# Performance work log

Measured on AMD Instinct MI355X. Metric: run time of the kernel, lower is better.

Reference implementation:

```python
import jax, jax.numpy as jnp
import numpy as np

N_NODES = 100000
DEG = 16
D_IN = 128
D_OUT = 128


def setup_inputs() -> dict:
    key = jax.random.key(0)
    k1, k2, k3, k4, k5, k6 = jax.random.split(key, 6)
    neighbours = jax.random.randint(k1, (N_NODES, DEG), 0, N_NODES, dtype=jnp.int64 if jax.config.jax_enable_x64 else jnp.int32)
    shape_features = jax.random.normal(k2, (N_NODES, D_IN), dtype=jnp.float32)
    scale = 1.0 / np.sqrt(D_IN)
    W1 = jax.random.normal(k3, (D_OUT, D_IN), dtype=jnp.float32) * scale
    b1 = jax.random.normal(k4, (D_OUT,), dtype=jnp.float32) * scale
    W2 = jax.random.normal(k5, (D_OUT, D_IN), dtype=jnp.float32) * scale
    b2 = jax.random.normal(k6, (D_OUT,), dtype=jnp.float32) * scale
    return {"neighbours": neighbours, "shape_features": shape_features,
            "W1": W1, "b1": b1, "W2": W2, "b2": b2}


def reference(neighbours, shape_features, W1, b1, W2, b2):
    # linear1(x): x @ W1^T + b1  -> [N, D_OUT]
    out1 = jnp.einsum('nd,od->no', shape_features, W1) + b1
    # per-node neighbor gather + sum (vectorized form of the Python loop)
    # gathered: [N, DEG, D_IN], aggr: [N, D_IN]
    aggr = shape_features[neighbours].sum(axis=1)
    out = out1 + jnp.einsum('nd,od->no', aggr, W2) + b2
    return jax.nn.relu(out)
```

## Files before the change

kernel.cpp:

```cpp
#include <hip/hip_runtime.h>
#include <stdint.h>


#define N_NODES 100000
#define DEG 16

typedef __attribute__((ext_vector_type(8))) short short8;
typedef __attribute__((ext_vector_type(4))) float floatx4;

static __device__ __forceinline__ unsigned short f2bf(float f) {
  union { float f; uint32_t u; } v; v.f = f;
  uint32_t u = v.u;
  return (unsigned short)((u + 0x7fffu + ((u >> 16) & 1u)) >> 16);
}
static __device__ __forceinline__ float bf2f(uint32_t bits16) {
  union { uint32_t u; float f; } v; v.u = bits16 << 16; return v.f;
}

__global__ __launch_bounds__(256) void k_convert(const float* __restrict__ x,
                                                 unsigned short* __restrict__ Xb,
                                                 const float* __restrict__ W1, const float* __restrict__ b1,
                                                 const float* __restrict__ W2, const float* __restrict__ b2,
                                                 unsigned short* __restrict__ Bt, float* __restrict__ bias) {
  int b = blockIdx.x;
  if (b < 12500) {
    int t = b * 256 + threadIdx.x;
    int n = t >> 5, c4 = t & 31;
    float4 v = *(const float4*)(x + (size_t)n * 128 + (size_t)c4 * 4);
    ushort4 o;
    o.x = f2bf(v.x); o.y = f2bf(v.y); o.z = f2bf(v.z); o.w = f2bf(v.w);
    *(ushort4*)(Xb + (size_t)n * 128 + (size_t)c4 * 4) = o;
  } else {
    int t = (b - 12500) * 256 + threadIdx.x;
    int o = t >> 8, k = t & 255;
    float v = (k < 128) ? W1[o * 128 + k] : W2[o * 128 + (k - 128)];
    Bt[t] = f2bf(v);
    if (t < 128) bias[t] = b1[t] + b2[t];
  }
}

__global__ __launch_bounds__(256, 8) void k_fused(const int* __restrict__ nbrs,
                                                  const unsigned short* __restrict__ Xb,
                                                  const unsigned short* __restrict__ Bt,
                                                  const float* __restrict__ bias,
                                                  float* __restrict__ out) {
  __shared__ uint4 aggr4[512];
  char* aggr = (char*)aggr4;
  const int tid = threadIdx.x;
  const int lane = tid & 63;
  const int w = tid >> 6;
  const int q16 = lane >> 4, c16 = lane & 15;
  const int tile = blockIdx.x * 32;
  const char* Xbb = (const char*)Xb;
  const char* Btb = (const char*)Bt;

  float bcol[2];
#pragma unroll
  for (int ni = 0; ni < 2; ++ni) bcol[ni] = bias[w * 32 + ni * 16 + c16];

  int base = (tile + w * 8) * DEG;
  int midx0 = nbrs[base + lane];
  int midx1 = nbrs[base + 64 + lane];

  for (int q = 0; q < 8; ++q) {
    int midx = (q < 4) ? midx0 : midx1;
    int flat = (q & 3) * 16 + q16;
    float a8[8] = {0.f, 0.f, 0.f, 0.f, 0.f, 0.f, 0.f, 0.f};
#pragma unroll
    for (int i = 0; i < 4; ++i) {
      int nb = __shfl(midx, flat + i * 4);
      uint4 pv = *(const uint4*)(Xbb + (size_t)nb * 256 + c16 * 16);
      a8[0] += bf2f(pv.x & 0xffffu); a8[1] += bf2f(pv.x >> 16);
      a8[2] += bf2f(pv.y & 0xffffu); a8[3] += bf2f(pv.y >> 16);
      a8[4] += bf2f(pv.z & 0xffffu); a8[5] += bf2f(pv.z >> 16);
      a8[6] += bf2f(pv.w & 0xffffu); a8[7] += bf2f(pv.w >> 16);
    }
#pragma unroll
    for (int k = 0; k < 8; ++k) {
      a8[k] += __shfl_xor(a8[k], 16);
      a8[k] += __shfl_xor(a8[k], 32);
    }
    if (lane < 16) {
      int row = w * 8 + q;
      uint4 wv;
      wv.x = (uint32_t)f2bf(a8[0]) | ((uint32_t)f2bf(a8[1]) << 16);
      wv.y = (uint32_t)f2bf(a8[2]) | ((uint32_t)f2bf(a8[3]) << 16);
      wv.z = (uint32_t)f2bf(a8[4]) | ((uint32_t)f2bf(a8[5]) << 16);
      wv.w = (uint32_t)f2bf(a8[6]) | ((uint32_t)f2bf(a8[7]) << 16);
      *(uint4*)(aggr + row * 256 + ((c16 ^ (row & 7)) * 16)) = wv;
    }
  }

  __syncthreads();

  floatx4 acc[2][2];
#pragma unroll
  for (int mi = 0; mi < 2; ++mi)
#pragma unroll
    for (int ni = 0; ni < 2; ++ni) acc[mi][ni] = (floatx4){0.f, 0.f, 0.f, 0.f};

#pragma unroll
  for (int kt = 0; kt < 8; ++kt) {
    short8 a[2], b[2];
#pragma unroll
    for (int mi = 0; mi < 2; ++mi) {
      int row = mi * 16 + c16;
      if (kt < 4) {
        a[mi] = *(const short8*)(Xbb + (size_t)(tile + row) * 256 + kt * 64 + q16 * 16);
      } else {
        int slot = (((kt - 4) * 4 + q16) ^ (row & 7)) * 16;
        a[mi] = *(const short8*)(aggr + row * 256 + slot);
      }
    }
#pragma unroll
    for (int ni = 0; ni < 2; ++ni) {
      int o = w * 32 + ni * 16 + c16;
      b[ni] = *(const short8*)(Btb + (size_t)o * 512 + kt * 64 + q16 * 16);
    }
    __builtin_amdgcn_s_setprio(1);
    acc[0][0] = __builtin_amdgcn_mfma_f32_16x16x32_bf16(a[0], b[0], acc[0][0], 0, 0, 0);
    acc[0][1] = __builtin_amdgcn_mfma_f32_16x16x32_bf16(a[0], b[1], acc[0][1], 0, 0, 0);
    acc[1][0] = __builtin_amdgcn_mfma_f32_16x16x32_bf16(a[1], b[0], acc[1][0], 0, 0, 0);
    acc[1][1] = __builtin_amdgcn_mfma_f32_16x16x32_bf16(a[1], b[1], acc[1][1], 0, 0, 0);
    __builtin_amdgcn_s_setprio(0);
  }

#pragma unroll
  for (int mi = 0; mi < 2; ++mi) {
    int rbase = tile + mi * 16 + q16 * 4;
#pragma unroll
    for (int r = 0; r < 4; ++r) {
      float* orow = out + (size_t)(rbase + r) * 128 + w * 32 + c16;
#pragma unroll
      for (int ni = 0; ni < 2; ++ni) {
        float vv = acc[mi][ni][r] + bcol[ni];
        orow[ni * 16] = vv > 0.f ? vv : 0.f;
      }
    }
  }
}

extern "C" void kernel_launch(void* const* d_in, const int* in_sizes, int n_in,
                              void* d_out, int out_size, void* d_ws, size_t ws_size,
                              hipStream_t stream) {
  const int* nbrs  = (const int*)d_in[0];
  const float* x   = (const float*)d_in[1];
  const float* W1  = (const float*)d_in[2];
  const float* b1  = (const float*)d_in[3];
  const float* W2  = (const float*)d_in[4];
  const float* b2  = (const float*)d_in[5];
  float* out = (float*)d_out;

  unsigned short* Xb = (unsigned short*)d_ws;
  unsigned short* Bt = Xb + (size_t)N_NODES * 128;
  float* bias = (float*)(Bt + 128 * 256);

  k_convert<<<12628, 256, 0, stream>>>(x, Xb, W1, b1, W2, b2, Bt, bias);
  k_fused<<<3125, 256, 0, stream>>>(nbrs, Xb, Bt, bias, out);
}
```

Baseline: 177.9 us.

## Double-buffer neighbour gathers and stage self tile into LDS via async loads

Software-pipelines the neighbour gather by issuing the next quad's global loads into one register buffer while summing the previous one. It also copies the block's own 32-row X tile into a swizzled LDS buffer with global_load_lds at kernel start, so the MFMA loop reads A operands from LDS instead of global memory. The occupancy hint drops from 8 to 6 blocks per CU to make room for the extra registers and the doubled LDS, which can reduce latency hiding across waves.

Result: faster. 170.6 us (-4.1%).

```diff
diff --git a/kernel.cpp b/kernel.cpp
--- a/kernel.cpp
+++ b/kernel.cpp
@@ -39,13 +39,14 @@
   }
 }
 
-__global__ __launch_bounds__(256, 8) void k_fused(const int* __restrict__ nbrs,
+__global__ __launch_bounds__(256, 6) void k_fused(const int* __restrict__ nbrs,
                                                   const unsigned short* __restrict__ Xb,
                                                   const unsigned short* __restrict__ Bt,
                                                   const float* __restrict__ bias,
                                                   float* __restrict__ out) {
-  __shared__ uint4 aggr4[512];
-  char* aggr = (char*)aggr4;
+  __shared__ uint4 lds4[1024];
+  char* xbuf = (char*)lds4;
+  char* aggr = (char*)lds4 + 8192;
   const int tid = threadIdx.x;
   const int lane = tid & 63;
   const int w = tid >> 6;
@@ -53,6 +54,16 @@
   const int tile = blockIdx.x * 32;
   const char* Xbb = (const char*)Xb;
   const char* Btb = (const char*)Bt;
+
+#pragma unroll
+  for (int i = 0; i < 2; ++i) {
+    int g = w * 2 + i;
+    int row = 4 * g + (lane >> 4);
+    const char* src = Xbb + (size_t)(tile + row) * 256 + ((size_t)((lane & 15) ^ (row & 7))) * 16;
+    __builtin_amdgcn_global_load_lds((const __attribute__((address_space(1))) uint32_t*)src,
+                                     (__attribute__((address_space(3))) uint32_t*)(xbuf + g * 1024),
+                                     16, 0, 0);
+  }
 
   float bcol[2];
 #pragma unroll
@@ -62,14 +73,21 @@
   int midx0 = nbrs[base + lane];
   int midx1 = nbrs[base + 64 + lane];
 
-  for (int q = 0; q < 8; ++q) {
+  uint4 pA[4], pB[4];
+  auto ISSUE = [&](int q, uint4* buf) {
     int midx = (q < 4) ? midx0 : midx1;
     int flat = (q & 3) * 16 + q16;
+#pragma unroll
+    for (int i = 0; i < 4; ++i) {
+      int nb = __shfl(midx, flat + i * 4);
+      buf[i] = *(const uint4*)(Xbb + (size_t)nb * 256 + c16 * 16);
+    }
+  };
+  auto CONSUME = [&](int q, uint4* buf) {
     float a8[8] = {0.f, 0.f, 0.f, 0.f, 0.f, 0.f, 0.f, 0.f};
 #pragma unroll
     for (int i = 0; i < 4; ++i) {
-      int nb = __shfl(midx, flat + i * 4);
-      uint4 pv = *(const uint4*)(Xbb + (size_t)nb * 256 + c16 * 16);
+      uint4 pv = buf[i];
       a8[0] += bf2f(pv.x & 0xffffu); a8[1] += bf2f(pv.x >> 16);
       a8[2] += bf2f(pv.y & 0xffffu); a8[3] += bf2f(pv.y >> 16);
       a8[4] += bf2f(pv.z & 0xffffu); a8[5] += bf2f(pv.z >> 16);
@@ -89,7 +107,17 @@
       wv.w = (uint32_t)f2bf(a8[6]) | ((uint32_t)f2bf(a8[7]) << 16);
       *(uint4*)(aggr + row * 256 + ((c16 ^ (row & 7)) * 16)) = wv;
     }
-  }
+  };
+
+  ISSUE(0, pA);
+  ISSUE(1, pB); CONSUME(0, pA);
+  ISSUE(2, pA); CONSUME(1, pB);
+  ISSUE(3, pB); CONSUME(2, pA);
+  ISSUE(4, pA); CONSUME(3, pB);
+  ISSUE(5, pB); CONSUME(4, pA);
+  ISSUE(6, pA); CONSUME(5, pB);
+  ISSUE(7, pB); CONSUME(6, pA);
+  CONSUME(7, pB);
 
   __syncthreads();
 
@@ -101,16 +129,13 @@
 
 #pragma unroll
   for (int kt = 0; kt < 8; ++kt) {
+    const char* srcb = (kt < 4) ? xbuf : aggr;
+    int s = (kt & 3) * 4 + q16;
     short8 a[2], b[2];
 #pragma unroll
     for (int mi = 0; mi < 2; ++mi) {
       int row = mi * 16 + c16;
-      if (kt < 4) {
-        a[mi] = *(const short8*)(Xbb + (size_t)(tile + row) * 256 + kt * 64 + q16 * 16);
-      } else {
-        int slot = (((kt - 4) * 4 + q16) ^ (row & 7)) * 16;
-        a[mi] = *(const short8*)(aggr + row * 256 + slot);
-      }
+      a[mi] = *(const short8*)(srcb + row * 256 + ((s ^ (row & 7)) * 16));
     }
 #pragma unroll
     for (int ni = 0; ni < 2; ++ni) {
```

## Assign one node per 16-lane group in gather, dropping cross-lane reductions

Applied to the files above, without the earlier changes.

The neighbour gather now gives each 16-lane group a whole node and has it walk all 16 neighbours, instead of splitting one node's neighbours across four groups and combining partial sums with shuffles. This removes the xor-shuffle reductions and the lane<16 guarded writes, so all lanes store rows to shared memory. The high bf16 half is now unpacked with a mask instead of shift-then-shift. The trade-off is a longer serial chain of 16 loads per lane (two rounds instead of eight), which relies on memory-level parallelism from unrolling and may raise register pressure.

Measured after the change: 182.8 us. 1.03x slower.

```diff
diff --git a/kernel.cpp b/kernel.cpp
--- a/kernel.cpp
+++ b/kernel.cpp
@@ -13,8 +13,11 @@
   uint32_t u = v.u;
   return (unsigned short)((u + 0x7fffu + ((u >> 16) & 1u)) >> 16);
 }
-static __device__ __forceinline__ float bf2f(uint32_t bits16) {
-  union { uint32_t u; float f; } v; v.u = bits16 << 16; return v.f;
+static __device__ __forceinline__ float bflo(uint32_t u) {
+  union { uint32_t u; float f; } v; v.u = u << 16; return v.f;
+}
+static __device__ __forceinline__ float bfhi(uint32_t u) {
+  union { uint32_t u; float f; } v; v.u = u & 0xffff0000u; return v.f;
 }
 
 __global__ __launch_bounds__(256) void k_convert(const float* __restrict__ x,
@@ -49,7 +52,7 @@
   const int tid = threadIdx.x;
   const int lane = tid & 63;
   const int w = tid >> 6;
-  const int q16 = lane >> 4, c16 = lane & 15;
+  const int g = lane >> 4, c16 = lane & 15;
   const int tile = blockIdx.x * 32;
   const char* Xbb = (const char*)Xb;
   const char* Btb = (const char*)Bt;
@@ -58,37 +61,27 @@
 #pragma unroll
   for (int ni = 0; ni < 2; ++ni) bcol[ni] = bias[w * 32 + ni * 16 + c16];
 
-  int base = (tile + w * 8) * DEG;
-  int midx0 = nbrs[base + lane];
-  int midx1 = nbrs[base + 64 + lane];
-
-  for (int q = 0; q < 8; ++q) {
-    int midx = (q < 4) ? midx0 : midx1;
-    int flat = (q & 3) * 16 + q16;
+  const int nbase = (tile + w * 8) * DEG;
+#pragma unroll
+  for (int round = 0; round < 2; ++round) {
+    int midx = nbrs[nbase + round * 64 + lane];
     float a8[8] = {0.f, 0.f, 0.f, 0.f, 0.f, 0.f, 0.f, 0.f};
 #pragma unroll
-    for (int i = 0; i < 4; ++i) {
-      int nb = __shfl(midx, flat + i * 4);
+    for (int j = 0; j < DEG; ++j) {
+      int nb = __shfl(midx, g * 16 + j);
       uint4 pv = *(const uint4*)(Xbb + (size_t)nb * 256 + c16 * 16);
-      a8[0] += bf2f(pv.x & 0xffffu); a8[1] += bf2f(pv.x >> 16);
-      a8[2] += bf2f(pv.y & 0xffffu); a8[3] += bf2f(pv.y >> 16);
-      a8[4] += bf2f(pv.z & 0xffffu); a8[5] += bf2f(pv.z >> 16);
-      a8[6] += bf2f(pv.w & 0xffffu); a8[7] += bf2f(pv.w >> 16);
+      a8[0] += bflo(pv.x); a8[1] += bfhi(pv.x);
+      a8[2] += bflo(pv.y); a8[3] += bfhi(pv.y);
+      a8[4] += bflo(pv.z); a8[5] += bfhi(pv.z);
+      a8[6] += bflo(pv.w); a8[7] += bfhi(pv.w);
     }
-#pragma unroll
-    for (int k = 0; k < 8; ++k) {
-      a8[k] += __shfl_xor(a8[k], 16);
-      a8[k] += __shfl_xor(a8[k], 32);
-    }
-    if (lane < 16) {
-      int row = w * 8 + q;
-      uint4 wv;
-      wv.x = (uint32_t)f2bf(a8[0]) | ((uint32_t)f2bf(a8[1]) << 16);
-      wv.y = (uint32_t)f2bf(a8[2]) | ((uint32_t)f2bf(a8[3]) << 16);
-      wv.z = (uint32_t)f2bf(a8[4]) | ((uint32_t)f2bf(a8[5]) << 16);
-      wv.w = (uint32_t)f2bf(a8[6]) | ((uint32_t)f2bf(a8[7]) << 16);
-      *(uint4*)(aggr + row * 256 + ((c16 ^ (row & 7)) * 16)) = wv;
-    }
+    int row = w * 8 + round * 4 + g;
+    uint4 wv;
+    wv.x = (uint32_t)f2bf(a8[0]) | ((uint32_t)f2bf(a8[1]) << 16);
+    wv.y = (uint32_t)f2bf(a8[2]) | ((uint32_t)f2bf(a8[3]) << 16);
+    wv.z = (uint32_t)f2bf(a8[4]) | ((uint32_t)f2bf(a8[5]) << 16);
+    wv.w = (uint32_t)f2bf(a8[6]) | ((uint32_t)f2bf(a8[7]) << 16);
+    *(uint4*)(aggr + row * 256 + ((c16 ^ (row & 7)) * 16)) = wv;
   }
 
   __syncthreads();
@@ -106,16 +99,16 @@
     for (int mi = 0; mi < 2; ++mi) {
       int row = mi * 16 + c16;
       if (kt < 4) {
-        a[mi] = *(const short8*)(Xbb + (size_t)(tile + row) * 256 + kt * 64 + q16 * 16);
+        a[mi] = *(const short8*)(Xbb + (size_t)(tile + row) * 256 + kt * 64 + g * 16);
       } else {
-        int slot = (((kt - 4) * 4 + q16) ^ (row & 7)) * 16;
+        int slot = (((kt - 4) * 4 + g) ^ (row & 7)) * 16;
         a[mi] = *(const short8*)(aggr + row * 256 + slot);
       }
     }
 #pragma unroll
     for (int ni = 0; ni < 2; ++ni) {
       int o = w * 32 + ni * 16 + c16;
-      b[ni] = *(const short8*)(Btb + (size_t)o * 512 + kt * 64 + q16 * 16);
+      b[ni] = *(const short8*)(Btb + (size_t)o * 512 + kt * 64 + g * 16);
     }
     __builtin_amdgcn_s_setprio(1);
     acc[0][0] = __builtin_amdgcn_mfma_f32_16x16x32_bf16(a[0], b[0], acc[0][0], 0, 0, 0);
@@ -127,7 +120,7 @@
 
 #pragma unroll
   for (int mi = 0; mi < 2; ++mi) {
-    int rbase = tile + mi * 16 + q16 * 4;
+    int rbase = tile + mi * 16 + g * 4;
 #pragma unroll
     for (int r = 0; r < 4; ++r) {
       float* orow = out + (size_t)(rbase + r) * 128 + w * 32 + c16;
```

## Give each wave its own 16-row tile and drop block-level barrier

Applied to the files above, without the earlier changes.

Each wave now owns 16 output rows across all 128 output columns, with a private LDS slice for its aggregated neighbour rows. This removes the block-wide __syncthreads between the gather and MFMA phases, and each A fragment is reused across 8 MFMAs instead of 2. Blocks now cover 64 rows, so half as many blocks are launched, and occupancy is capped at 6 blocks per CU. The cost is that every wave reloads the full weight matrix from global or cache, and each wave holds more accumulator registers.

Measured after the change: 220.8 us. 1.24x slower.

```diff
diff --git a/kernel.cpp b/kernel.cpp
--- a/kernel.cpp
+++ b/kernel.cpp
@@ -39,103 +39,85 @@
   }
 }
 
-__global__ __launch_bounds__(256, 8) void k_fused(const int* __restrict__ nbrs,
+__global__ __launch_bounds__(256, 6) void k_fused(const int* __restrict__ nbrs,
                                                   const unsigned short* __restrict__ Xb,
                                                   const unsigned short* __restrict__ Bt,
                                                   const float* __restrict__ bias,
                                                   float* __restrict__ out) {
-  __shared__ uint4 aggr4[512];
-  char* aggr = (char*)aggr4;
+  __shared__ uint4 lds4[1024];
   const int tid = threadIdx.x;
   const int lane = tid & 63;
   const int w = tid >> 6;
-  const int q16 = lane >> 4, c16 = lane & 15;
-  const int tile = blockIdx.x * 32;
+  const int g = lane >> 4, c16 = lane & 15;
+  const int rb = blockIdx.x * 64 + w * 16;
+  if (rb >= N_NODES) return;
+  char* aggr = (char*)(lds4 + w * 256);
   const char* Xbb = (const char*)Xb;
   const char* Btb = (const char*)Bt;
 
-  float bcol[2];
+  float bcol[8];
 #pragma unroll
-  for (int ni = 0; ni < 2; ++ni) bcol[ni] = bias[w * 32 + ni * 16 + c16];
+  for (int nt = 0; nt < 8; ++nt) bcol[nt] = bias[nt * 16 + c16];
 
-  int base = (tile + w * 8) * DEG;
-  int midx0 = nbrs[base + lane];
-  int midx1 = nbrs[base + 64 + lane];
-
-  for (int q = 0; q < 8; ++q) {
-    int midx = (q < 4) ? midx0 : midx1;
-    int flat = (q & 3) * 16 + q16;
-    float a8[8] = {0.f, 0.f, 0.f, 0.f, 0.f, 0.f, 0.f, 0.f};
+  for (int qq = 0; qq < 4; ++qq) {
+    int mi_ = nbrs[(size_t)rb * DEG + qq * 64 + lane];
+    for (int qi = 0; qi < 4; ++qi) {
+      int q = qq * 4 + qi;
+      float a8[8] = {0.f, 0.f, 0.f, 0.f, 0.f, 0.f, 0.f, 0.f};
 #pragma unroll
-    for (int i = 0; i < 4; ++i) {
-      int nb = __shfl(midx, flat + i * 4);
-      uint4 pv = *(const uint4*)(Xbb + (size_t)nb * 256 + c16 * 16);
-      a8[0] += bf2f(pv.x & 0xffffu); a8[1] += bf2f(pv.x >> 16);
-      a8[2] += bf2f(pv.y & 0xffffu); a8[3] += bf2f(pv.y >> 16);
-      a8[4] += bf2f(pv.z & 0xffffu); a8[5] += bf2f(pv.z >> 16);
-      a8[6] += bf2f(pv.w & 0xffffu); a8[7] += bf2f(pv.w >> 16);
-    }
+      for (int i = 0; i < 4; ++i) {
+        int nb = __shfl(mi_, qi * 16 + i * 4 + g);
+        uint4 pv = *(const uint4*)(Xbb + (size_t)nb * 256 + c16 * 16);
+        a8[0] += bf2f(pv.x & 0xffffu); a8[1] += bf2f(pv.x >> 16);
+        a8[2] += bf2f(pv.y & 0xffffu); a8[3] += bf2f(pv.y >> 16);
+        a8[4] += bf2f(pv.z & 0xffffu); a8[5] += bf2f(pv.z >> 16);
+        a8[6] += bf2f(pv.w & 0xffffu); a8[7] += bf2f(pv.w >> 16);
+      }
 #pragma unroll
-    for (int k = 0; k < 8; ++k) {
-      a8[k] += __shfl_xor(a8[k], 16);
-      a8[k] += __shfl_xor(a8[k], 32);
-    }
-    if (lane < 16) {
-      int row = w * 8 + q;
-      uint4 wv;
-      wv.x = (uint32_t)f2bf(a8[0]) | ((uint32_t)f2bf(a8[1]) << 16);
-      wv.y = (uint32_t)f2bf(a8[2]) | ((uint32_t)f2bf(a8[3]) << 16);
-      wv.z = (uint32_t)f2bf(a8[4]) | ((uint32_t)f2bf(a8[5]) << 16);
-      wv.w = (uint32_t)f2bf(a8[6]) | ((uint32_t)f2bf(a8[7]) << 16);
-      *(uint4*)(aggr + row * 256 + ((c16 ^ (row & 7)) * 16)) = wv;
+      for (int k = 0; k < 8; ++k) {
+        a8[k] += __shfl_xor(a8[k], 16);
+        a8[k] += __shfl_xor(a8[k], 32);
+      }
+      if (lane < 16) {
+        uint4 wv;
+        wv.x = (uint32_t)f2bf(a8[0]) | ((uint32_t)f2bf(a8[1]) << 16);
+        wv.y = (uint32_t)f2bf(a8[2]) | ((uint32_t)f2bf(a8[3]) << 16);
+        wv.z = (uint32_t)f2bf(a8[4]) | ((uint32_t)f2bf(a8[5]) << 16);
+        wv.w = (uint32_t)f2bf(a8[6]) | ((uint32_t)f2bf(a8[7]) << 16);
+        *(uint4*)(aggr + q * 256 + ((c16 ^ (q & 7)) * 16)) = wv;
+      }
     }
   }
 
-  __syncthreads();
-
-  floatx4 acc[2][2];
+  floatx4 acc[8];
 #pragma unroll
-  for (int mi = 0; mi < 2; ++mi)
-#pragma unroll
-    for (int ni = 0; ni < 2; ++ni) acc[mi][ni] = (floatx4){0.f, 0.f, 0.f, 0.f};
+  for (int nt = 0; nt < 8; ++nt) acc[nt] = (floatx4){0.f, 0.f, 0.f, 0.f};
 
 #pragma unroll
   for (int kt = 0; kt < 8; ++kt) {
-    short8 a[2], b[2];
-#pragma unroll
-    for (int mi = 0; mi < 2; ++mi) {
-      int row = mi * 16 + c16;
-      if (kt < 4) {
-        a[mi] = *(const short8*)(Xbb + (size_t)(tile + row) * 256 + kt * 64 + q16 * 16);
-      } else {
-        int slot = (((kt - 4) * 4 + q16) ^ (row & 7)) * 16;
-        a[mi] = *(const short8*)(aggr + row * 256 + slot);
-      }
-    }
-#pragma unroll
-    for (int ni = 0; ni < 2; ++ni) {
-      int o = w * 32 + ni * 16 + c16;
-      b[ni] = *(const short8*)(Btb + (size_t)o * 512 + kt * 64 + q16 * 16);
+    short8 a;
+    if (kt < 4) {
+      a = *(const short8*)(Xbb + (size_t)(rb + c16) * 256 + kt * 64 + g * 16);
+    } else {
+      int slot = (((kt - 4) * 4 + g) ^ (c16 & 7)) * 16;
+      a = *(const short8*)(aggr + c16 * 256 + slot);
     }
     __builtin_amdgcn_s_setprio(1);
-    acc[0][0] = __builtin_amdgcn_mfma_f32_16x16x32_bf16(a[0], b[0], acc[0][0], 0, 0, 0);
-    acc[0][1] = __builtin_amdgcn_mfma_f32_16x16x32_bf16(a[0], b[1], acc[0][1], 0, 0, 0);
-    acc[1][0] = __builtin_amdgcn_mfma_f32_16x16x32_bf16(a[1], b[0], acc[1][0], 0, 0, 0);
-    acc[1][1] = __builtin_amdgcn_mfma_f32_16x16x32_bf16(a[1], b[1], acc[1][1], 0, 0, 0);
+#pragma unroll
+    for (int nt = 0; nt < 8; ++nt) {
+      short8 b = *(const short8*)(Btb + (size_t)(nt * 16 + c16) * 512 + kt * 64 + g * 16);
+      acc[nt] = __builtin_amdgcn_mfma_f32_16x16x32_bf16(a, b, acc[nt], 0, 0, 0);
+    }
     __builtin_amdgcn_s_setprio(0);
   }
 
 #pragma unroll
-  for (int mi = 0; mi < 2; ++mi) {
-    int rbase = tile + mi * 16 + q16 * 4;
+  for (int r = 0; r < 4; ++r) {
+    float* orow = out + (size_t)(rb + g * 4 + r) * 128 + c16;
 #pragma unroll
-    for (int r = 0; r < 4; ++r) {
-      float* orow = out + (size_t)(rbase + r) * 128 + w * 32 + c16;
-#pragma unroll
-      for (int ni = 0; ni < 2; ++ni) {
-        float vv = acc[mi][ni][r] + bcol[ni];
-        orow[ni * 16] = vv > 0.f ? vv : 0.f;
-      }
+    for (int nt = 0; nt < 8; ++nt) {
+      float vv = acc[nt][r] + bcol[nt];
+      orow[nt * 16] = vv > 0.f ? vv : 0.f;
     }
   }
 }
@@ -156,5 +138,5 @@
   float* bias = (float*)(Bt + 128 * 256);
 
   k_convert<<<12628, 256, 0, stream>>>(x, Xb, W1, b1, W2, b2, Bt, bias);
-  k_fused<<<3125, 256, 0, stream>>>(nbrs, Xb, Bt, bias, out);
+  k_fused<<<1563, 256, 0, stream>>>(nbrs, Xb, Bt, bias, out);
 }
```
